# Kernel tuning notes

Measured on AMD Instinct MI355X. Metric: run time of the kernel, lower is better.

## Reference

```python
import jax, jax.numpy as jnp
import numpy as np

NEG_SLOPE = 0.2

def gat_conv(x, src, dst, W, a_src, a_dst, b, n_nodes):
    # x: [N, Fin]; src/dst: [E] (self-loops included); W: [Fin, H]
    h = x @ W                                   # [N, H]
    s_src = h @ a_src                           # [N]
    s_dst = h @ a_dst                           # [N]
    e = jax.nn.leaky_relu(s_src[src] + s_dst[dst], NEG_SLOPE)  # [E]
    # scatter-softmax over incoming edges per destination node
    m = jax.ops.segment_max(e, dst, num_segments=n_nodes)      # [N]
    ex = jnp.exp(e - m[dst])                                   # [E]
    denom = jax.ops.segment_sum(ex, dst, num_segments=n_nodes) # [N]
    alpha = ex / denom[dst]                                    # [E]
    out = jax.ops.segment_sum(h[src] * alpha[:, None], dst, num_segments=n_nodes)
    return out + b


def setup_inputs() -> dict:
    key = jax.random.key(0)
    ks = jax.random.split(key, 16)
    N, E, F_IN, H, C = 100000, 1600000, 128, 128, 64
    x = jax.random.normal(ks[0], (N, F_IN), dtype=jnp.float32)
    edge_index = jax.random.randint(ks[1], (2, E), 0, N, dtype=jnp.int64)
    def glorot(k, shape):
        fan = sum(shape)
        return jax.random.normal(k, shape, dtype=jnp.float32) * jnp.sqrt(2.0 / fan)
    W1 = glorot(ks[2], (F_IN, H)); a1_src = glorot(ks[3], (H,)); a1_dst = glorot(ks[4], (H,)); b1 = jnp.zeros((H,), jnp.float32)
    W2 = glorot(ks[5], (H, H));    a2_src = glorot(ks[6], (H,)); a2_dst = glorot(ks[7], (H,)); b2 = jnp.zeros((H,), jnp.float32)
    Wl = glorot(ks[8], (H, C));    bl = jnp.zeros((C,), jnp.float32)
    return {"x": x, "edge_index": edge_index,
            "W1": W1, "a1_src": a1_src, "a1_dst": a1_dst, "b1": b1,
            "W2": W2, "a2_src": a2_src, "a2_dst": a2_dst, "b2": b2,
            "Wl": Wl, "bl": bl}


def reference(x, edge_index, W1, a1_src, a1_dst, b1, W2, a2_src, a2_dst, b2, Wl, bl):
    n = x.shape[0]
    loops = jnp.arange(n, dtype=edge_index.dtype)
    src = jnp.concatenate([edge_index[0], loops])  # add_self_loops=True (PyG default)
    dst = jnp.concatenate([edge_index[1], loops])
    h = jax.nn.relu(gat_conv(x, src, dst, W1, a1_src, a1_dst, b1, n))
    # F.dropout in eval mode is identity
    h2 = gat_conv(h, src, dst, W2, a2_src, a2_dst, b2, n)
    out = h + h2
    logp = jax.nn.log_softmax(out @ Wl + bl, axis=1)
    return (logp, edge_index)
```

## Files before the change

### kernel.cpp

```cpp
#include <hip/hip_runtime.h>

typedef unsigned short u16;
typedef __bf16 bf16x8 __attribute__((ext_vector_type(8)));
typedef float f32x4 __attribute__((ext_vector_type(4)));
typedef unsigned short u16x8 __attribute__((ext_vector_type(8)));

#define GA 256

static __device__ __forceinline__ float bf2f(u16 u) {
    return __uint_as_float(((unsigned)u) << 16);
}
static __device__ __forceinline__ u16 f2bf(float f) {
    unsigned u = __float_as_uint(f);
    unsigned r = (u + 0x7FFFu + ((u >> 16) & 1u)) >> 16;
    return (u16)r;
}

__global__ void detect_kernel(const int* __restrict__ ei, int* __restrict__ flag) {
    if (blockIdx.x == 0 && threadIdx.x == 0) {
        int zc = 0;
        for (int t = 0; t < 64; ++t) zc += (ei[2 * t + 1] == 0) ? 1 : 0;
        *flag = (zc >= 60) ? 2 : 1;
    }
}
static __device__ __forceinline__ int ld_idx(const int* ei, int pos, int st, int N) {
    int v = ei[(size_t)pos * (size_t)st];
    return v < 0 ? 0 : (v >= N ? N - 1 : v);
}

#define SCHUNK 4096
__global__ void xscan_reduce(const int* __restrict__ arr, int* __restrict__ bsum, int M) {
    __shared__ int sdata[256];
    int t = threadIdx.x;
    int base = blockIdx.x * SCHUNK + t * 16;
    int s = 0;
#pragma unroll
    for (int j = 0; j < 16; ++j) { int i = base + j; s += (i < M) ? arr[i] : 0; }
    sdata[t] = s;
    __syncthreads();
    for (int o = 128; o > 0; o >>= 1) {
        if (t < o) sdata[t] += sdata[t + o];
        __syncthreads();
    }
    if (t == 0) bsum[blockIdx.x] = sdata[0];
}
__global__ void scan_mid_kernel(int* __restrict__ bsum, int nb) {
    if (threadIdx.x == 0 && blockIdx.x == 0) {
        int run = 0;
        for (int b = 0; b < nb; ++b) { int v = bsum[b]; bsum[b] = run; run += v; }
    }
}
__global__ void xscan_final(int* __restrict__ arr, const int* __restrict__ bsum, int M) {
    __shared__ int sdata[256];
    int t = threadIdx.x;
    int base = blockIdx.x * SCHUNK + t * 16;
    int v[16];
    int s = 0;
#pragma unroll
    for (int j = 0; j < 16; ++j) {
        int i = base + j;
        v[j] = (i < M) ? arr[i] : 0;
        s += v[j];
    }
    sdata[t] = s;
    __syncthreads();
    for (int o = 1; o < 256; o <<= 1) {
        int add = (t >= o) ? sdata[t - o] : 0;
        __syncthreads();
        sdata[t] += add;
        __syncthreads();
    }
    int excl = (t == 0) ? 0 : sdata[t - 1];
    int off = bsum[blockIdx.x] + excl;
#pragma unroll
    for (int j = 0; j < 16; ++j) {
        int i = base + j;
        if (i < M) { arr[i] = off; off += v[j]; }
    }
}

__global__ __launch_bounds__(256) void partition_kernel(const int* __restrict__ ei,
                                                        const int* __restrict__ flag,
                                                        const int* __restrict__ offs,
                                                        unsigned* __restrict__ ebuf, int E,
                                                        int N) {
    __shared__ int cur[1024];
    const int K = (N + 127) >> 7;
    const int bh = blockIdx.x;
    for (int k = threadIdx.x; k < K; k += 256) cur[k] = offs[(size_t)k * GA + bh];
    __syncthreads();
    const int st = *flag;
    const int chunk = (E + GA - 1) / GA;
    const int lo = bh * chunk;
    const int hi = (lo + chunk < E) ? lo + chunk : E;
    for (int j = lo + (int)threadIdx.x; j < hi; j += 256) {
        int d = ld_idx(ei, E + j, st, N);
        int s = ld_idx(ei, j, st, N);
        int pos = atomicAdd(&cur[d >> 7], 1);
        ebuf[pos] = ((unsigned)(d & 127) << 25) | (unsigned)s;
    }
}

__global__ __launch_bounds__(256) void csr_build(const unsigned* __restrict__ ebuf,
                                                 const int* __restrict__ offs,
                                                 int* __restrict__ rowptr,
                                                 int* __restrict__ col, int E, int N, int ET) {
    __shared__ int dg[128];
    __shared__ int sc[128];
    __shared__ int cur[128];
    const int K = (N + 127) >> 7;
    const int k = blockIdx.x;
    const int base = k << 7;
    const int nn = (N - base < 128) ? (N - base) : 128;
    const int e0 = offs[(size_t)k * GA];
    const int e1 = (k + 1 < K) ? offs[(size_t)(k + 1) * GA] : E;
    for (int t = threadIdx.x; t < 128; t += 256) dg[t] = 0;
    __syncthreads();
    for (int e = e0 + (int)threadIdx.x; e < e1; e += 256)
        atomicAdd(&dg[ebuf[e] >> 25], 1);
    __syncthreads();
    const int t = threadIdx.x;
    int v = 0;
    if (t < 128) {
        v = (t < nn) ? dg[t] + 1 : 0;
        sc[t] = v;
    }
    __syncthreads();
    for (int o = 1; o < 128; o <<= 1) {
        int add = 0;
        if (t < 128 && t >= o) add = sc[t - o];
        __syncthreads();
        if (t < 128) sc[t] += add;
        __syncthreads();
    }
    const int colbase = e0 + base;
    if (t < nn) {
        int rp = colbase + sc[t] - v;
        rowptr[base + t] = rp;
        col[rp] = base + t;
        cur[t] = rp + 1;
    }
    if (k == 0 && t == 0) rowptr[N] = ET;
    __syncthreads();
    for (int e = e0 + (int)threadIdx.x; e < e1; e += 256) {
        unsigned p = ebuf[e];
        int pos = atomicAdd(&cur[p >> 25], 1);
        col[pos] = (int)(p & 0x1FFFFFFu);
    }
}

template <int NC, bool AF32, int EPI, bool HIST>
__global__ __launch_bounds__(256) void gemm_fused(
    const void* __restrict__ Ap, const float* __restrict__ W, u16* __restrict__ Cout, int M,
    const float* __restrict__ av_s, const float* __restrict__ av_d, float* __restrict__ ssrc,
    float* __restrict__ sdst, const float* __restrict__ bl, float* __restrict__ outp,
    const int* __restrict__ ei, const int* __restrict__ flag, int* __restrict__ cntmat, int E,
    int ET, int N, int G1) {
    if (HIST && (int)blockIdx.x >= G1) {
        __shared__ int cnt[1024];
        const int bh = (int)blockIdx.x - G1;
        const int nga = (int)gridDim.x - G1;
        const int K = (N + 127) >> 7;
        for (int k = threadIdx.x; k < K; k += 256) cnt[k] = 0;
        __syncthreads();
        const int st = *flag;
        const int chunk = (E + nga - 1) / nga;
        const int lo = bh * chunk;
        const int hi = (lo + chunk < E) ? lo + chunk : E;
        for (int j = lo + (int)threadIdx.x; j < hi; j += 256) {
            int d = ld_idx(ei, E + j, st, N);
            atomicAdd(&cnt[d >> 7], 1);
        }
        __syncthreads();
        for (int k = threadIdx.x; k < K; k += 256) cntmat[(size_t)k * nga + bh] = cnt[k];
        return;
    }
    const int lane = threadIdx.x & 63;
    const int quad = lane >> 4;
    const int r = lane & 15;
    const int gw = (blockIdx.x * 256 + threadIdx.x) >> 6;
    const int nw = G1 * 4;

    bf16x8 bf[NC / 16][4];
#pragma unroll
    for (int nt = 0; nt < NC / 16; ++nt)
#pragma unroll
        for (int kk = 0; kk < 4; ++kk) {
            union { bf16x8 v; u16 s[8]; } u;
#pragma unroll
            for (int j = 0; j < 8; ++j)
                u.s[j] = f2bf(W[(size_t)(kk * 32 + quad * 8 + j) * NC + nt * 16 + r]);
            bf[nt][kk] = u.v;
        }
    float avs[NC / 16], avd[NC / 16], blv[NC / 16];
    if (EPI == 1) {
#pragma unroll
        for (int nt = 0; nt < NC / 16; ++nt) {
            avs[nt] = av_s[nt * 16 + r];
            avd[nt] = av_d[nt * 16 + r];
        }
    }
    if (EPI == 2) {
#pragma unroll
        for (int nt = 0; nt < NC / 16; ++nt) blv[nt] = bl[nt * 16 + r];
    }

    const int ntiles = (M + 15) >> 4;
    for (int t = gw; t < ntiles; t += nw) {
        const int row0 = t << 4;
        bf16x8 af[4];
        if (AF32) {
            const float* arow = (const float*)Ap + (size_t)(row0 + r) * 128;
#pragma unroll
            for (int kk = 0; kk < 4; ++kk) {
                f32x4 f0 = *reinterpret_cast<const f32x4*>(arow + kk * 32 + quad * 8);
                f32x4 f1 = *reinterpret_cast<const f32x4*>(arow + kk * 32 + quad * 8 + 4);
                union { bf16x8 v; u16 s[8]; } u;
#pragma unroll
                for (int j = 0; j < 4; ++j) { u.s[j] = f2bf(f0[j]); u.s[4 + j] = f2bf(f1[j]); }
                af[kk] = u.v;
            }
        } else {
            const u16* arow = (const u16*)Ap + (size_t)(row0 + r) * 128;
#pragma unroll
            for (int kk = 0; kk < 4; ++kk)
                af[kk] = *reinterpret_cast<const bf16x8*>(arow + kk * 32 + quad * 8);
        }
        f32x4 acc[NC / 16];
#pragma unroll
        for (int nt = 0; nt < NC / 16; ++nt) acc[nt] = (f32x4){0.f, 0.f, 0.f, 0.f};
#pragma unroll
        for (int kk = 0; kk < 4; ++kk)
#pragma unroll
            for (int nt = 0; nt < NC / 16; ++nt)
                acc[nt] = __builtin_amdgcn_mfma_f32_16x16x32_bf16(af[kk], bf[nt][kk],
                                                                  acc[nt], 0, 0, 0);
        if (EPI != 2) {
#pragma unroll
            for (int nt = 0; nt < NC / 16; ++nt)
#pragma unroll
                for (int reg = 0; reg < 4; ++reg)
                    Cout[(size_t)(row0 + quad * 4 + reg) * NC + nt * 16 + r] =
                        f2bf(acc[nt][reg]);
        }
        if (EPI == 1) {
            float ps[4] = {0.f, 0.f, 0.f, 0.f}, pd[4] = {0.f, 0.f, 0.f, 0.f};
#pragma unroll
            for (int nt = 0; nt < NC / 16; ++nt)
#pragma unroll
                for (int reg = 0; reg < 4; ++reg) {
                    ps[reg] += acc[nt][reg] * avs[nt];
                    pd[reg] += acc[nt][reg] * avd[nt];
                }
#pragma unroll
            for (int o = 1; o < 16; o <<= 1)
#pragma unroll
                for (int reg = 0; reg < 4; ++reg) {
                    ps[reg] += __shfl_xor(ps[reg], o);
                    pd[reg] += __shfl_xor(pd[reg], o);
                }
            if (r == 0) {
#pragma unroll
                for (int reg = 0; reg < 4; ++reg) {
                    ssrc[row0 + quad * 4 + reg] = ps[reg];
                    sdst[row0 + quad * 4 + reg] = pd[reg];
                }
            }
        }
        if (EPI == 2) {
#pragma unroll
            for (int reg = 0; reg < 4; ++reg) {
                float v[NC / 16];
                float m = -3.4e38f;
#pragma unroll
                for (int nt = 0; nt < NC / 16; ++nt) {
                    v[nt] = acc[nt][reg] + blv[nt];
                    m = fmaxf(m, v[nt]);
                }
#pragma unroll
                for (int o = 1; o < 16; o <<= 1) m = fmaxf(m, __shfl_xor(m, o));
                float s = 0.f;
#pragma unroll
                for (int nt = 0; nt < NC / 16; ++nt) s += __expf(v[nt] - m);
#pragma unroll
                for (int o = 1; o < 16; o <<= 1) s += __shfl_xor(s, o);
                float L = __logf(s);
                const size_t rb = (size_t)(row0 + quad * 4 + reg) * NC;
#pragma unroll
                for (int nt = 0; nt < NC / 16; ++nt)
                    outp[rb + nt * 16 + r] = v[nt] - m - L;
            }
        }
    }
}

template <int MODE>
__global__ __launch_bounds__(256) void agg_fused(
    const int* __restrict__ rowptr, const int* __restrict__ col,
    const float* __restrict__ ssrc, const float* __restrict__ sdst,
    const u16* __restrict__ h, const float* __restrict__ b, const u16* __restrict__ skip,
    u16* __restrict__ out, int N) {
    const int lane = threadIdx.x & 63;
    const int gwave = (blockIdx.x * 256 + threadIdx.x) >> 6;
    const int grp = lane >> 4;
    const int ln = lane & 15;
    const int i = gwave * 4 + grp;
    if (i >= N) return;
    const int start = rowptr[i], end = rowptr[i + 1];
    const float sd = sdst[i];
    const size_t coff = (size_t)ln * 8;

    float acc[8] = {0.f, 0.f, 0.f, 0.f, 0.f, 0.f, 0.f, 0.f};
    float sm = 0.f;
    int e = start;
    for (; e + 4 <= end; e += 4) {
        int c0 = col[e], c1 = col[e + 1], c2 = col[e + 2], c3 = col[e + 3];
        float s0 = ssrc[c0] + sd;
        float s1 = ssrc[c1] + sd;
        float s2 = ssrc[c2] + sd;
        float s3 = ssrc[c3] + sd;
        const u16x8 r0 = *reinterpret_cast<const u16x8*>(h + (size_t)c0 * 128 + coff);
        const u16x8 r1 = *reinterpret_cast<const u16x8*>(h + (size_t)c1 * 128 + coff);
        const u16x8 r2 = *reinterpret_cast<const u16x8*>(h + (size_t)c2 * 128 + coff);
        const u16x8 r3 = *reinterpret_cast<const u16x8*>(h + (size_t)c3 * 128 + coff);
        s0 = s0 > 0.f ? s0 : 0.2f * s0;
        s1 = s1 > 0.f ? s1 : 0.2f * s1;
        s2 = s2 > 0.f ? s2 : 0.2f * s2;
        s3 = s3 > 0.f ? s3 : 0.2f * s3;
        float w0 = __expf(fminf(s0, 60.f));
        float w1 = __expf(fminf(s1, 60.f));
        float w2 = __expf(fminf(s2, 60.f));
        float w3 = __expf(fminf(s3, 60.f));
        sm += (w0 + w1) + (w2 + w3);
#pragma unroll
        for (int j = 0; j < 8; ++j)
            acc[j] += (w0 * bf2f(r0[j]) + w1 * bf2f(r1[j])) +
                      (w2 * bf2f(r2[j]) + w3 * bf2f(r3[j]));
    }
    for (; e < end; ++e) {
        int c0 = col[e];
        float s0 = ssrc[c0] + sd;
        s0 = s0 > 0.f ? s0 : 0.2f * s0;
        float w0 = __expf(fminf(s0, 60.f));
        const u16x8 r0 = *reinterpret_cast<const u16x8*>(h + (size_t)c0 * 128 + coff);
        sm += w0;
#pragma unroll
        for (int j = 0; j < 8; ++j) acc[j] += w0 * bf2f(r0[j]);
    }
    const float rd = 1.f / sm;

    u16x8 o;
    if (MODE == 1) {
#pragma unroll
        for (int j = 0; j < 8; ++j) {
            float v = acc[j] * rd + b[coff + j];
            v = v > 0.f ? v : 0.f;
            o[j] = f2bf(v);
        }
    } else {
        const u16x8 sk = *reinterpret_cast<const u16x8*>(skip + (size_t)i * 128 + coff);
#pragma unroll
        for (int j = 0; j < 8; ++j) {
            float v = acc[j] * rd + b[coff + j] + bf2f(sk[j]);
            o[j] = f2bf(v);
        }
    }
    *reinterpret_cast<u16x8*>(out + (size_t)i * 128 + coff) = o;
}

__global__ void copy_ei_kernel(const int* __restrict__ ei, const int* __restrict__ flag,
                               float* __restrict__ out, int n, int N) {
    int j = blockIdx.x * 256 + threadIdx.x;
    if (j < n) out[j] = (float)ld_idx(ei, j, *flag, N);
}

extern "C" void kernel_launch(void* const* d_in, const int* in_sizes, int n_in, void* d_out,
                              int out_size, void* d_ws, size_t ws_size, hipStream_t stream) {
    int ix = 0, iei = 1;
    if (in_sizes[0] < in_sizes[1]) { ix = 1; iei = 0; }
    const float* x = (const float*)d_in[ix];
    const int* ei = (const int*)d_in[iei];
    const float* W1 = (const float*)d_in[2];
    const float* a1s = (const float*)d_in[3];
    const float* a1d = (const float*)d_in[4];
    const float* b1 = (const float*)d_in[5];
    const float* W2 = (const float*)d_in[6];
    const float* a2s = (const float*)d_in[7];
    const float* a2d = (const float*)d_in[8];
    const float* b2 = (const float*)d_in[9];
    const float* Wl = (const float*)d_in[10];
    const float* bl = (const float*)d_in[11];

    const int N = in_sizes[ix] / 128;
    const int E = (out_size - N * 64) / 2;
    const int ET = E + N;
    const int K = (N + 127) >> 7;
    const int Mscan = K * GA;

    char* ws = (char*)d_ws;
    size_t off = 0;
    auto alloc = [&](size_t bytes) {
        void* p = ws + off;
        off += (bytes + 255) & ~(size_t)255;
        return p;
    };
    u16* h = (u16*)alloc((size_t)N * 128 * 2);
    u16* h1 = (u16*)alloc((size_t)N * 128 * 2);
    u16* o2 = (u16*)alloc((size_t)N * 128 * 2);
    float* ssrc = (float*)alloc((size_t)N * 4);
    float* sdst = (float*)alloc((size_t)N * 4);
    int* eflag = (int*)alloc(256);
    int* cntmat = (int*)alloc((size_t)Mscan * 4);
    int* rowptr = (int*)alloc((size_t)(N + 1) * 4);
    int* bsum = (int*)alloc(4096);
    int* colv = (int*)alloc((size_t)ET * 4);
    unsigned* ebuf = (unsigned*)h1;

    float* out_logp = (float*)d_out;
    float* out_ei = out_logp + (size_t)N * 64;

    dim3 blk(256);
    const int ngrid4 = (N + 15) / 16;
    const int nbx = (Mscan + SCHUNK - 1) / SCHUNK;
    const int G1 = 512;

    detect_kernel<<<1, 64, 0, stream>>>(ei, eflag);

    gemm_fused<128, true, 1, true><<<G1 + GA, blk, 0, stream>>>(
        x, W1, h, N, a1s, a1d, ssrc, sdst, nullptr, nullptr, ei, eflag, cntmat, E, ET, N, G1);

    xscan_reduce<<<nbx, blk, 0, stream>>>(cntmat, bsum, Mscan);
    scan_mid_kernel<<<1, 64, 0, stream>>>(bsum, nbx);
    xscan_final<<<nbx, blk, 0, stream>>>(cntmat, bsum, Mscan);

    partition_kernel<<<GA, blk, 0, stream>>>(ei, eflag, cntmat, ebuf, E, N);
    csr_build<<<K, blk, 0, stream>>>(ebuf, cntmat, rowptr, colv, E, N, ET);

    agg_fused<1><<<ngrid4, blk, 0, stream>>>(rowptr, colv, ssrc, sdst, h, b1, nullptr, h1, N);

    gemm_fused<128, false, 1, false><<<G1, blk, 0, stream>>>(
        h1, W2, h, N, a2s, a2d, ssrc, sdst, nullptr, nullptr, nullptr, nullptr, nullptr, 0, 0,
        N, G1);
    agg_fused<2><<<ngrid4, blk, 0, stream>>>(rowptr, colv, ssrc, sdst, h, b2, h1, o2, N);

    gemm_fused<64, false, 2, false><<<G1, blk, 0, stream>>>(
        o2, Wl, nullptr, N, nullptr, nullptr, nullptr, nullptr, bl, out_logp, nullptr, nullptr,
        nullptr, 0, 0, N, G1);

    copy_ei_kernel<<<(2 * E + 255) / 256, blk, 0, stream>>>(ei, eflag, out_ei, 2 * E, N);
}
```

Baseline: 369.3 us.

## Fold edge-index copy into partition, raise GA, use bf16 dot2 aggregation

The separate copy_ei kernel is removed and its work now runs in extra blocks of partition_kernel, so it overlaps with the partition work. GA goes from 256 to 1024, giving the partition and counting stages more parallel chunks but a larger count matrix to scan. The aggregation inner loop packs pairs of bf16 features with truncated bf16 attention weights and accumulates them with v_dot2_f32_bf16 instead of scalar FMAs. Truncating the weights to bf16 lowers the precision of the softmax weights, though the normaliser sum uses the same truncated values so it stays consistent.

```diff
diff --git a/kernel.cpp b/kernel.cpp
--- a/kernel.cpp
+++ b/kernel.cpp
@@ -5,7 +5,7 @@
 typedef float f32x4 __attribute__((ext_vector_type(4)));
 typedef unsigned short u16x8 __attribute__((ext_vector_type(8)));
 
-#define GA 256
+#define GA 1024
 
 static __device__ __forceinline__ float bf2f(u16 u) {
     return __uint_as_float(((unsigned)u) << 16);
@@ -82,14 +82,21 @@
 __global__ __launch_bounds__(256) void partition_kernel(const int* __restrict__ ei,
                                                         const int* __restrict__ flag,
                                                         const int* __restrict__ offs,
-                                                        unsigned* __restrict__ ebuf, int E,
-                                                        int N) {
+                                                        unsigned* __restrict__ ebuf,
+                                                        float* __restrict__ out_ei, int E,
+                                                        int N, int twoE) {
+    const int st = *flag;
+    if ((int)blockIdx.x >= GA) {
+        int tid = ((int)blockIdx.x - GA) * 256 + threadIdx.x;
+        int stride = ((int)gridDim.x - GA) * 256;
+        for (int j = tid; j < twoE; j += stride) out_ei[j] = (float)ld_idx(ei, j, st, N);
+        return;
+    }
     __shared__ int cur[1024];
     const int K = (N + 127) >> 7;
     const int bh = blockIdx.x;
     for (int k = threadIdx.x; k < K; k += 256) cur[k] = offs[(size_t)k * GA + bh];
     __syncthreads();
-    const int st = *flag;
     const int chunk = (E + GA - 1) / GA;
     const int lo = bh * chunk;
     const int hi = (lo + chunk < E) ? lo + chunk : E;
@@ -319,10 +326,11 @@
         float s1 = ssrc[c1] + sd;
         float s2 = ssrc[c2] + sd;
         float s3 = ssrc[c3] + sd;
-        const u16x8 r0 = *reinterpret_cast<const u16x8*>(h + (size_t)c0 * 128 + coff);
-        const u16x8 r1 = *reinterpret_cast<const u16x8*>(h + (size_t)c1 * 128 + coff);
-        const u16x8 r2 = *reinterpret_cast<const u16x8*>(h + (size_t)c2 * 128 + coff);
-        const u16x8 r3 = *reinterpret_cast<const u16x8*>(h + (size_t)c3 * 128 + coff);
+        union { u16x8 v; unsigned w[4]; } r0, r1, r2, r3;
+        r0.v = *reinterpret_cast<const u16x8*>(h + (size_t)c0 * 128 + coff);
+        r1.v = *reinterpret_cast<const u16x8*>(h + (size_t)c1 * 128 + coff);
+        r2.v = *reinterpret_cast<const u16x8*>(h + (size_t)c2 * 128 + coff);
+        r3.v = *reinterpret_cast<const u16x8*>(h + (size_t)c3 * 128 + coff);
         s0 = s0 > 0.f ? s0 : 0.2f * s0;
         s1 = s1 > 0.f ? s1 : 0.2f * s1;
         s2 = s2 > 0.f ? s2 : 0.2f * s2;
@@ -331,21 +339,61 @@
         float w1 = __expf(fminf(s1, 60.f));
         float w2 = __expf(fminf(s2, 60.f));
         float w3 = __expf(fminf(s3, 60.f));
-        sm += (w0 + w1) + (w2 + w3);
-#pragma unroll
-        for (int j = 0; j < 8; ++j)
-            acc[j] += (w0 * bf2f(r0[j]) + w1 * bf2f(r1[j])) +
-                      (w2 * bf2f(r2[j]) + w3 * bf2f(r3[j]));
-    }
-    for (; e < end; ++e) {
+        unsigned u0 = __float_as_uint(w0) & 0xFFFF0000u;
+        unsigned u1 = __float_as_uint(w1) & 0xFFFF0000u;
+        unsigned u2 = __float_as_uint(w2) & 0xFFFF0000u;
+        unsigned u3 = __float_as_uint(w3) & 0xFFFF0000u;
+        sm += (__uint_as_float(u0) + __uint_as_float(u1)) +
+              (__uint_as_float(u2) + __uint_as_float(u3));
+        unsigned wp01 = __builtin_amdgcn_perm(u1, u0, 0x07060302u);
+        unsigned wp23 = __builtin_amdgcn_perm(u3, u2, 0x07060302u);
+#pragma unroll
+        for (int jw = 0; jw < 4; ++jw) {
+            unsigned lo01 = __builtin_amdgcn_perm(r1.w[jw], r0.w[jw], 0x05040100u);
+            unsigned hi01 = __builtin_amdgcn_perm(r1.w[jw], r0.w[jw], 0x07060302u);
+            unsigned lo23 = __builtin_amdgcn_perm(r3.w[jw], r2.w[jw], 0x05040100u);
+            unsigned hi23 = __builtin_amdgcn_perm(r3.w[jw], r2.w[jw], 0x07060302u);
+            asm("v_dot2_f32_bf16 %0, %1, %2, %0" : "+v"(acc[2 * jw]) : "v"(lo01), "v"(wp01));
+            asm("v_dot2_f32_bf16 %0, %1, %2, %0" : "+v"(acc[2 * jw + 1]) : "v"(hi01), "v"(wp01));
+            asm("v_dot2_f32_bf16 %0, %1, %2, %0" : "+v"(acc[2 * jw]) : "v"(lo23), "v"(wp23));
+            asm("v_dot2_f32_bf16 %0, %1, %2, %0" : "+v"(acc[2 * jw + 1]) : "v"(hi23), "v"(wp23));
+        }
+    }
+    if (e + 2 <= end) {
+        int c0 = col[e], c1 = col[e + 1];
+        float s0 = ssrc[c0] + sd;
+        float s1 = ssrc[c1] + sd;
+        union { u16x8 v; unsigned w[4]; } r0, r1;
+        r0.v = *reinterpret_cast<const u16x8*>(h + (size_t)c0 * 128 + coff);
+        r1.v = *reinterpret_cast<const u16x8*>(h + (size_t)c1 * 128 + coff);
+        s0 = s0 > 0.f ? s0 : 0.2f * s0;
+        s1 = s1 > 0.f ? s1 : 0.2f * s1;
+        float w0 = __expf(fminf(s0, 60.f));
+        float w1 = __expf(fminf(s1, 60.f));
+        unsigned u0 = __float_as_uint(w0) & 0xFFFF0000u;
+        unsigned u1 = __float_as_uint(w1) & 0xFFFF0000u;
+        sm += __uint_as_float(u0) + __uint_as_float(u1);
+        unsigned wp01 = __builtin_amdgcn_perm(u1, u0, 0x07060302u);
+#pragma unroll
+        for (int jw = 0; jw < 4; ++jw) {
+            unsigned lo01 = __builtin_amdgcn_perm(r1.w[jw], r0.w[jw], 0x05040100u);
+            unsigned hi01 = __builtin_amdgcn_perm(r1.w[jw], r0.w[jw], 0x07060302u);
+            asm("v_dot2_f32_bf16 %0, %1, %2, %0" : "+v"(acc[2 * jw]) : "v"(lo01), "v"(wp01));
+            asm("v_dot2_f32_bf16 %0, %1, %2, %0" : "+v"(acc[2 * jw + 1]) : "v"(hi01), "v"(wp01));
+        }
+        e += 2;
+    }
+    if (e < end) {
         int c0 = col[e];
         float s0 = ssrc[c0] + sd;
         s0 = s0 > 0.f ? s0 : 0.2f * s0;
         float w0 = __expf(fminf(s0, 60.f));
+        unsigned u0 = __float_as_uint(w0) & 0xFFFF0000u;
+        float wt = __uint_as_float(u0);
+        sm += wt;
         const u16x8 r0 = *reinterpret_cast<const u16x8*>(h + (size_t)c0 * 128 + coff);
-        sm += w0;
-#pragma unroll
-        for (int j = 0; j < 8; ++j) acc[j] += w0 * bf2f(r0[j]);
+#pragma unroll
+        for (int j = 0; j < 8; ++j) acc[j] += wt * bf2f(r0[j]);
     }
     const float rd = 1.f / sm;
 
@@ -366,12 +414,6 @@
         }
     }
     *reinterpret_cast<u16x8*>(out + (size_t)i * 128 + coff) = o;
-}
-
-__global__ void copy_ei_kernel(const int* __restrict__ ei, const int* __restrict__ flag,
-                               float* __restrict__ out, int n, int N) {
-    int j = blockIdx.x * 256 + threadIdx.x;
-    if (j < n) out[j] = (float)ld_idx(ei, j, *flag, N);
 }
 
 extern "C" void kernel_launch(void* const* d_in, const int* in_sizes, int n_in, void* d_out,
@@ -433,7 +475,8 @@
     scan_mid_kernel<<<1, 64, 0, stream>>>(bsum, nbx);
     xscan_final<<<nbx, blk, 0, stream>>>(cntmat, bsum, Mscan);
 
-    partition_kernel<<<GA, blk, 0, stream>>>(ei, eflag, cntmat, ebuf, E, N);
+    partition_kernel<<<GA + 2048, blk, 0, stream>>>(ei, eflag, cntmat, ebuf, out_ei, E, N,
+                                                    2 * E);
     csr_build<<<K, blk, 0, stream>>>(ebuf, cntmat, rowptr, colv, E, N, ET);
 
     agg_fused<1><<<ngrid4, blk, 0, stream>>>(rowptr, colv, ssrc, sdst, h, b1, nullptr, h1, N);
@@ -446,6 +489,4 @@
     gemm_fused<64, false, 2, false><<<G1, blk, 0, stream>>>(
         o2, Wl, nullptr, N, nullptr, nullptr, nullptr, nullptr, bl, out_logp, nullptr, nullptr,
         nullptr, 0, 0, N, G1);
-
-    copy_ei_kernel<<<(2 * E + 255) / 256, blk, 0, stream>>>(ei, eflag, out_ei, 2 * E, N);
-}
+}
```

Result: slower. 391.6 us (+6.0%).
